# Performance work log

Measured on AMD Instinct MI355X. Metric: run time of the kernel, lower is better.

Reference implementation:

```python
import jax, jax.numpy as jnp
import numpy as np

N_NODES = 10000
N_GRAPHS = 64
NEG_SLOPE = 0.2
EPS = 1e-16


def gat_conv(x, src, dst, W, a_src, a_dst, bias, heads, out_ch, num_nodes):
    """PyG GATConv (shared lin, add_self_loops already applied to src/dst)."""
    xl = (x @ W).reshape(num_nodes, heads, out_ch)          # [N,H,C]
    alpha_s = jnp.einsum('nhc,hc->nh', xl, a_src)           # [N,H]
    alpha_d = jnp.einsum('nhc,hc->nh', xl, a_dst)           # [N,H]
    e = jax.nn.leaky_relu(alpha_s[src] + alpha_d[dst], NEG_SLOPE)  # [E,H]
    # segment softmax over incoming edges of each destination node
    emax = jax.ops.segment_max(e, dst, num_segments=num_nodes)
    emax = jnp.where(jnp.isfinite(emax), emax, 0.0)
    ee = jnp.exp(e - emax[dst])
    denom = jax.ops.segment_sum(ee, dst, num_segments=num_nodes)
    alpha = ee / (denom[dst] + EPS)                         # [E,H]
    msg = xl[src] * alpha[:, :, None]                       # [E,H,C]
    out = jax.ops.segment_sum(msg, dst, num_segments=num_nodes)  # [N,H,C]
    return out.reshape(num_nodes, heads * out_ch) + bias


def setup_inputs() -> dict:
    key = jax.random.key(0)
    ks = jax.random.split(key, 16)
    H, C, IN = 8, 128, 128
    x = jax.random.normal(ks[0], (N_NODES, IN), jnp.float32)
    edge_index = jax.random.randint(ks[1], (2, 320000), 0, N_NODES, jnp.int64)
    batch = jnp.sort(jax.random.randint(ks[2], (N_NODES,), 0, N_GRAPHS, jnp.int64))
    g = lambda k, shp, fan: jax.random.normal(k, shp, jnp.float32) * (1.0 / np.sqrt(fan))
    return {
        'x': x, 'edge_index': edge_index, 'batch': batch,
        'W1': g(ks[3], (IN, H * C), IN),
        'a_src1': g(ks[4], (H, C), C), 'a_dst1': g(ks[5], (H, C), C),
        'b1': jnp.zeros((H * C,), jnp.float32),
        'W2': g(ks[6], (H * C, C), H * C),
        'a_src2': g(ks[7], (1, C), C), 'a_dst2': g(ks[8], (1, C), C),
        'b2': jnp.zeros((C,), jnp.float32),
        'lin1_w': g(ks[9], (C, 128), C), 'lin1_b': jnp.zeros((128,), jnp.float32),
        'lin2_w': g(ks[10], (128, 1), 128), 'lin2_b': jnp.zeros((1,), jnp.float32),
    }


def reference(x, edge_index, batch, W1, a_src1, a_dst1, b1, W2, a_src2, a_dst2, b2,
              lin1_w, lin1_b, lin2_w, lin2_b):
    loops = jnp.arange(N_NODES, dtype=edge_index.dtype)
    src = jnp.concatenate([edge_index[0], loops])
    dst = jnp.concatenate([edge_index[1], loops])
    h = jax.nn.elu(gat_conv(x, src, dst, W1, a_src1, a_dst1, b1, 8, 128, N_NODES))
    h = jax.nn.elu(gat_conv(h, src, dst, W2, a_src2, a_dst2, b2, 1, 128, N_NODES))
    # global mean pool over graphs
    sums = jax.ops.segment_sum(h, batch, num_segments=N_GRAPHS)
    cnts = jax.ops.segment_sum(jnp.ones((N_NODES,), h.dtype), batch, num_segments=N_GRAPHS)
    pooled = sums / jnp.maximum(cnts, 1.0)[:, None]         # [G,128]
    z = jax.nn.relu(pooled @ lin1_w + lin1_b)
    return (z @ lin2_w + lin2_b).squeeze(1)                 # [G]
```

## Files before the change

kernel.cpp:

```cpp
#include <hip/hip_runtime.h>
#include <math.h>

#define N_NODES 10000
#define N_GRAPHS 64
#define E_RAW 320000
#define E_ALL (E_RAW + N_NODES)
#define NEG_SLOPE 0.2f
#define EPS 1e-16f
#define CAP 192

typedef unsigned short ushort_t;
typedef short short8 __attribute__((ext_vector_type(8)));
typedef float floatx4 __attribute__((ext_vector_type(4)));

static __device__ __forceinline__ float bfl(unsigned u) {
  union { unsigned u; float f; } v; v.u = u << 16; return v.f;
}
static __device__ __forceinline__ float bfh(unsigned u) {
  union { unsigned u; float f; } v; v.u = u & 0xFFFF0000u; return v.f;
}
static __device__ __forceinline__ ushort_t f2bf(float f) {
  union { float f; unsigned u; } v; v.f = f;
  unsigned r = v.u + 0x7FFFu + ((v.u >> 16) & 1u);
  return (ushort_t)(r >> 16);
}

static __device__ __forceinline__ void load16_lds(const ushort_t* gp, ushort_t* ldsbase, int lane) {
#if __has_builtin(__builtin_amdgcn_global_load_lds)
  __builtin_amdgcn_global_load_lds((const __attribute__((address_space(1))) void*)gp,
                                   (__attribute__((address_space(3))) void*)ldsbase, 16, 0, 0);
#else
  *(uint4*)(ldsbase + lane * 8) = *(const uint4*)gp;
#endif
}

static __device__ __forceinline__ void swz_one(const float* __restrict__ W,
                                               ushort_t* __restrict__ Wsw,
                                               int idx, int K, int N) {
  int NT = N >> 4;
  int lane = idx & 63, tile = idx >> 6;
  int nt = tile % NT, kt = tile / NT;
  int n = nt * 16 + (lane & 15);
  int kb = kt * 32 + (lane >> 4) * 8;
  ushort4 lo, hi;
  lo.x = f2bf(W[(size_t)(kb + 0) * N + n]); lo.y = f2bf(W[(size_t)(kb + 1) * N + n]);
  lo.z = f2bf(W[(size_t)(kb + 2) * N + n]); lo.w = f2bf(W[(size_t)(kb + 3) * N + n]);
  hi.x = f2bf(W[(size_t)(kb + 4) * N + n]); hi.y = f2bf(W[(size_t)(kb + 5) * N + n]);
  hi.z = f2bf(W[(size_t)(kb + 6) * N + n]); hi.w = f2bf(W[(size_t)(kb + 7) * N + n]);
  *(ushort4*)(Wsw + (size_t)idx * 8) = lo;
  *(ushort4*)(Wsw + (size_t)idx * 8 + 4) = hi;
}

__global__ __launch_bounds__(1024) void prep_k(const float* __restrict__ x,
                                               const int* __restrict__ batch,
                                               const float* __restrict__ W1,
                                               const float* __restrict__ W2,
                                               const float* __restrict__ aS1,
                                               const float* __restrict__ aD1,
                                               ushort_t* __restrict__ xb,
                                               ushort_t* __restrict__ W1sw,
                                               ushort_t* __restrict__ W2sw,
                                               float* __restrict__ zero0,
                                               int* __restrict__ poolcnt,
                                               float* __restrict__ wAs,
                                               float* __restrict__ wAd) {
  __shared__ int shm[N_GRAPHS];
  const int b = blockIdx.x, t = threadIdx.x;
  if (b < 10) {
    int i4 = b * 1024 + t;
    if (i4 < 9548) *(float4*)(zero0 + i4 * 4) = make_float4(0.f, 0.f, 0.f, 0.f);
  } else if (b == 10) {
    if (t < N_GRAPHS) shm[t] = 0;
    __syncthreads();
    for (int n = t; n < N_NODES; n += 1024) atomicAdd(&shm[batch[n]], 1);
    __syncthreads();
    if (t < N_GRAPHS) poolcnt[t] = shm[t];
  } else if (b < 324) {
    int i4 = (b - 11) * 1024 + t;
    if (i4 < 320000) {
      float4 v = *(const float4*)(x + (size_t)i4 * 4);
      ushort4 o;
      o.x = f2bf(v.x); o.y = f2bf(v.y); o.z = f2bf(v.z); o.w = f2bf(v.w);
      *(ushort4*)(xb + (size_t)i4 * 4) = o;
    }
  } else if (b < 340) {
    int idx = (b - 324) * 1024 + t;
    if (idx < 16384) swz_one(W1, W1sw, idx, 128, 1024);
  } else if (b < 356) {
    int idx = (b - 340) * 1024 + t;
    if (idx < 16384) swz_one(W2, W2sw, idx, 1024, 128);
  } else {
    int h = t >> 7, k = t & 127;
    const float* wrow = W1 + (size_t)k * 1024 + h * 128;
    const float* as = aS1 + h * 128;
    const float* ad = aD1 + h * 128;
    float accS = 0.f, accD = 0.f;
    for (int c = 0; c < 128; c += 4) {
      float4 wv = *(const float4*)(wrow + c);
      float4 sv = *(const float4*)(as + c);
      float4 dv = *(const float4*)(ad + c);
      accS = fmaf(wv.x, sv.x, accS); accS = fmaf(wv.y, sv.y, accS);
      accS = fmaf(wv.z, sv.z, accS); accS = fmaf(wv.w, sv.w, accS);
      accD = fmaf(wv.x, dv.x, accD); accD = fmaf(wv.y, dv.y, accD);
      accD = fmaf(wv.z, dv.z, accD); accD = fmaf(wv.w, dv.w, accD);
    }
    wAs[h * 128 + k] = accS;
    wAd[h * 128 + k] = accD;
  }
}

__global__ __launch_bounds__(256) void lgf_k(const int* __restrict__ ei,
                                             int* __restrict__ degc,
                                             int* __restrict__ csr,
                                             const float* __restrict__ x,
                                             const float* __restrict__ wAs,
                                             const float* __restrict__ wAd,
                                             float* __restrict__ as1,
                                             float* __restrict__ ad1) {
  const int bid = blockIdx.x, t = threadIdx.x;
  if (bid < 1290) {
    int e = bid * 256 + t;
    if (e < E_ALL) {
      int s, d;
      if (e < E_RAW) { s = ei[e]; d = ei[E_RAW + e]; }
      else           { s = d = e - E_RAW; }
      int pos = atomicAdd(&degc[d], 1);
      if (pos < CAP) csr[d * CAP + pos] = s;
    }
    return;
  }
  int nb = bid - 1290;
  int n = nb * 16 + (t >> 4);
  int cb = t & 15, h = cb >> 1, sd = cb & 1;
  const float* w = (sd ? wAd : wAs) + h * 128;
  const float* xr = x + (size_t)n * 128;
  float acc = 0.f;
  for (int k = 0; k < 128; k += 4) {
    float4 xv = *(const float4*)(xr + k);
    float4 wv = *(const float4*)(w + k);
    acc = fmaf(xv.x, wv.x, acc); acc = fmaf(xv.y, wv.y, acc);
    acc = fmaf(xv.z, wv.z, acc); acc = fmaf(xv.w, wv.w, acc);
  }
  if (sd) ad1[n * 8 + h] = acc;
  else    as1[n * 8 + h] = acc;
}

__global__ __launch_bounds__(64) void agg1x_k(const ushort_t* __restrict__ xb,
                                              const float* __restrict__ as1,
                                              const float* __restrict__ ad1,
                                              const int* __restrict__ degc,
                                              const int* __restrict__ csr,
                                              ushort_t* __restrict__ aggx) {
  const int dst = blockIdx.x, t = threadIdx.x;
  int deg = degc[dst]; deg = deg < CAP ? deg : CAP;
  const int beg = dst * CAP;
  __shared__ unsigned offs[CAP];
  __shared__ float al[CAP][8];
  float ad[8];
  {
    float4 d0 = *(const float4*)(ad1 + dst * 8);
    float4 d1 = *(const float4*)(ad1 + dst * 8 + 4);
    ad[0] = d0.x; ad[1] = d0.y; ad[2] = d0.z; ad[3] = d0.w;
    ad[4] = d1.x; ad[5] = d1.y; ad[6] = d1.z; ad[7] = d1.w;
  }
  float pmax[8];
  #pragma unroll
  for (int h = 0; h < 8; h++) pmax[h] = -1e30f;
  for (int e = t; e < deg; e += 64) {
    int s = csr[beg + e];
    offs[e] = (unsigned)(s * 256);
    float4 a0 = *(const float4*)(as1 + s * 8);
    float4 a1 = *(const float4*)(as1 + s * 8 + 4);
    float lg[8] = {a0.x + ad[0], a0.y + ad[1], a0.z + ad[2], a0.w + ad[3],
                   a1.x + ad[4], a1.y + ad[5], a1.z + ad[6], a1.w + ad[7]};
    #pragma unroll
    for (int h = 0; h < 8; h++) {
      float v = lg[h]; v = v > 0.f ? v : NEG_SLOPE * v;
      al[e][h] = v;
      pmax[h] = fmaxf(pmax[h], v);
    }
  }
  #pragma unroll
  for (int h = 0; h < 8; h++) {
    #pragma unroll
    for (int off = 32; off; off >>= 1) pmax[h] = fmaxf(pmax[h], __shfl_xor(pmax[h], off));
  }
  float ps[8] = {};
  for (int e = t; e < deg; e += 64) {
    #pragma unroll
    for (int h = 0; h < 8; h++) {
      float ex = __expf(al[e][h] - pmax[h]);
      al[e][h] = ex;
      ps[h] += ex;
    }
  }
  #pragma unroll
  for (int h = 0; h < 8; h++) {
    #pragma unroll
    for (int off = 32; off; off >>= 1) ps[h] += __shfl_xor(ps[h], off);
    ps[h] = 1.0f / (ps[h] + EPS);
  }
  for (int e = t; e < deg; e += 64) {
    #pragma unroll
    for (int h = 0; h < 8; h++) al[e][h] *= ps[h];
  }
  const int degp = (deg + 3) & ~3;
  for (int e = deg + t; e < degp; e += 64) {
    offs[e] = 0;
    #pragma unroll
    for (int h = 0; h < 8; h++) al[e][h] = 0.f;
  }
  __syncthreads();
  const char* xbase = (const char*)xb;
  const unsigned toff = (unsigned)(4 * t);
  float aL[8] = {}, aH[8] = {};
  for (int e0 = 0; e0 < degp; e0 += 4) {
    #pragma unroll
    for (int j = 0; j < 4; j++) {
      int e = e0 + j;
      unsigned u = *(const unsigned*)(xbase + (offs[e] + toff));
      float4 q0 = *(const float4*)&al[e][0];
      float4 q1 = *(const float4*)&al[e][4];
      float lo = bfl(u), hi = bfh(u);
      aL[0] = fmaf(q0.x, lo, aL[0]); aH[0] = fmaf(q0.x, hi, aH[0]);
      aL[1] = fmaf(q0.y, lo, aL[1]); aH[1] = fmaf(q0.y, hi, aH[1]);
      aL[2] = fmaf(q0.z, lo, aL[2]); aH[2] = fmaf(q0.z, hi, aH[2]);
      aL[3] = fmaf(q0.w, lo, aL[3]); aH[3] = fmaf(q0.w, hi, aH[3]);
      aL[4] = fmaf(q1.x, lo, aL[4]); aH[4] = fmaf(q1.x, hi, aH[4]);
      aL[5] = fmaf(q1.y, lo, aL[5]); aH[5] = fmaf(q1.y, hi, aH[5]);
      aL[6] = fmaf(q1.z, lo, aL[6]); aH[6] = fmaf(q1.z, hi, aH[6]);
      aL[7] = fmaf(q1.w, lo, aL[7]); aH[7] = fmaf(q1.w, hi, aH[7]);
    }
  }
  ushort_t* op = aggx + (size_t)dst * 1024 + 2 * t;
  #pragma unroll
  for (int h = 0; h < 8; h++) {
    unsigned up = (unsigned)f2bf(aL[h]) | ((unsigned)f2bf(aH[h]) << 16);
    *(unsigned*)(op + h * 128) = up;
  }
}

__global__ __launch_bounds__(256) void gemm1h_k(const ushort_t* __restrict__ A,
                                                const ushort_t* __restrict__ Bsw,
                                                const float* __restrict__ b1,
                                                ushort_t* __restrict__ Cb) {
  __shared__ ushort_t Albuf[32 * 512];
  __shared__ float epi[4][16][68];
  const int bid = blockIdx.x, t = threadIdx.x;
  const int M = N_NODES, NT = 64;
  const int lane = t & 63, w = t >> 6;
  const int wm = w >> 1, wn = w & 1;
  const int m0 = (bid >> 3) * 128;
  const int h = bid & 7;
  const int g = lane >> 4, l16 = lane & 15;

  #pragma unroll
  for (int i = 0; i < 8; i++) {
    int tile = w * 8 + i;
    int mtl = tile >> 2, kt = tile & 3;
    int r = m0 + mtl * 16 + l16; r = r < M ? r : M - 1;
    load16_lds(A + ((size_t)r * 8 + h) * 128 + kt * 32 + g * 8, &Albuf[tile * 512], lane);
  }
  __syncthreads();

  floatx4 acc[4][4] = {};
  #pragma unroll
  for (int kt = 0; kt < 4; kt++) {
    short8 a[4], b[4];
    #pragma unroll
    for (int mi = 0; mi < 4; mi++)
      a[mi] = *(const short8*)&Albuf[(((wm * 4 + mi) * 4 + kt) * 64 + lane) * 8];
    #pragma unroll
    for (int ni = 0; ni < 4; ni++) {
      int nt = h * 8 + wn * 4 + ni;
      b[ni] = *(const short8*)(Bsw + ((size_t)(kt * NT + nt) * 64 + lane) * 8);
    }
    #pragma unroll
    for (int mi = 0; mi < 4; mi++)
      #pragma unroll
      for (int ni = 0; ni < 4; ni++)
        acc[mi][ni] = __builtin_amdgcn_mfma_f32_16x16x32_bf16(a[mi], b[ni], acc[mi][ni], 0, 0, 0);
  }

  const int r = lane >> 2, c0 = (lane & 3) * 16;
  const int colh = wn * 64 + c0;
  float bv[16];
  #pragma unroll
  for (int c = 0; c < 16; c++) bv[c] = b1[h * 128 + colh + c];
  #pragma unroll
  for (int mi = 0; mi < 4; mi++) {
    #pragma unroll
    for (int ni = 0; ni < 4; ni++)
      #pragma unroll
      for (int reg = 0; reg < 4; reg++)
        epi[w][g * 4 + reg][ni * 16 + l16] = acc[mi][ni][reg];
    float4 v0 = *(float4*)&epi[w][r][c0];
    float4 v1 = *(float4*)&epi[w][r][c0 + 4];
    float4 v2 = *(float4*)&epi[w][r][c0 + 8];
    float4 v3 = *(float4*)&epi[w][r][c0 + 12];
    float vr[16] = {v0.x,v0.y,v0.z,v0.w, v1.x,v1.y,v1.z,v1.w,
                    v2.x,v2.y,v2.z,v2.w, v3.x,v3.y,v3.z,v3.w};
    int grow = m0 + wm * 64 + mi * 16 + r;
    if (grow < M) {
      ushort_t hv[16];
      #pragma unroll
      for (int c = 0; c < 16; c++) {
        float v = vr[c] + bv[c];
        v = v > 0.f ? v : (__expf(v) - 1.0f);
        hv[c] = f2bf(v);
      }
      uint4 u0, u1;
      u0.x = (unsigned)hv[0] | ((unsigned)hv[1] << 16);
      u0.y = (unsigned)hv[2] | ((unsigned)hv[3] << 16);
      u0.z = (unsigned)hv[4] | ((unsigned)hv[5] << 16);
      u0.w = (unsigned)hv[6] | ((unsigned)hv[7] << 16);
      u1.x = (unsigned)hv[8] | ((unsigned)hv[9] << 16);
      u1.y = (unsigned)hv[10] | ((unsigned)hv[11] << 16);
      u1.z = (unsigned)hv[12] | ((unsigned)hv[13] << 16);
      u1.w = (unsigned)hv[14] | ((unsigned)hv[15] << 16);
      ushort_t* cp = Cb + (size_t)grow * 1024 + h * 128 + colh;
      *(uint4*)cp = u0;
      *(uint4*)(cp + 8) = u1;
    }
  }
}

__global__ __launch_bounds__(256) void gemm2_k(const ushort_t* __restrict__ A,
                                               const ushort_t* __restrict__ Bsw,
                                               ushort_t* __restrict__ Cb,
                                               const float* __restrict__ aS,
                                               const float* __restrict__ aD,
                                               float* __restrict__ asO,
                                               float* __restrict__ adO) {
  const int M = N_NODES, K = 1024, NT = 8;
  __shared__ ushort_t Albuf[4 * 512];
  __shared__ float epi[4][16][36];
  const int t = threadIdx.x, lane = t & 63, w = t >> 6;
  const int mb0 = blockIdx.x * 16;
  const int g = lane >> 4, l16 = lane & 15;

  floatx4 acc[2] = {};
  for (int ch = 0; ch < 8; ch++) {
    {
      int r = mb0 + l16; r = r < M ? r : M - 1;
      load16_lds(A + (size_t)r * K + (ch * 4 + w) * 32 + g * 8, &Albuf[w * 512], lane);
    }
    __syncthreads();
    #pragma unroll
    for (int ks = 0; ks < 4; ks++) {
      short8 a = *(const short8*)&Albuf[(ks * 64 + lane) * 8];
      #pragma unroll
      for (int ni = 0; ni < 2; ni++) {
        int nt = w * 2 + ni, ktg = ch * 4 + ks;
        short8 b = *(const short8*)(Bsw + ((size_t)(ktg * NT + nt) * 64 + lane) * 8);
        acc[ni] = __builtin_amdgcn_mfma_f32_16x16x32_bf16(a, b, acc[ni], 0, 0, 0);
      }
    }
    __syncthreads();
  }

  const int r = lane >> 2, c0 = (lane & 3) * 8;
  const int colh = w * 32 + c0;
  float asc[8], adc[8];
  #pragma unroll
  for (int c = 0; c < 8; c++) { asc[c] = aS[colh + c]; adc[c] = aD[colh + c]; }
  #pragma unroll
  for (int ni = 0; ni < 2; ni++)
    #pragma unroll
    for (int reg = 0; reg < 4; reg++)
      epi[w][g * 4 + reg][ni * 16 + l16] = acc[ni][reg];
  float4 v0 = *(float4*)&epi[w][r][c0];
  float4 v1 = *(float4*)&epi[w][r][c0 + 4];
  float vr[8] = {v0.x, v0.y, v0.z, v0.w, v1.x, v1.y, v1.z, v1.w};
  int grow = mb0 + r;
  float sp = 0.f, dp = 0.f;
  ushort_t hv[8];
  #pragma unroll
  for (int c = 0; c < 8; c++) {
    sp = fmaf(vr[c], asc[c], sp);
    dp = fmaf(vr[c], adc[c], dp);
    hv[c] = f2bf(vr[c]);
  }
  sp += __shfl_xor(sp, 1); sp += __shfl_xor(sp, 2);
  dp += __shfl_xor(dp, 1); dp += __shfl_xor(dp, 2);
  if (grow < M) {
    uint4 u0;
    u0.x = (unsigned)hv[0] | ((unsigned)hv[1] << 16);
    u0.y = (unsigned)hv[2] | ((unsigned)hv[3] << 16);
    u0.z = (unsigned)hv[4] | ((unsigned)hv[5] << 16);
    u0.w = (unsigned)hv[6] | ((unsigned)hv[7] << 16);
    *(uint4*)(Cb + (size_t)grow * 128 + colh) = u0;
    if ((lane & 3) == 0) {
      atomicAdd(&asO[grow], sp);
      atomicAdd(&adO[grow], dp);
    }
  }
}

__global__ __launch_bounds__(64) void agg2_k(const ushort_t* __restrict__ xlb2,
                                             const float* __restrict__ as2,
                                             const float* __restrict__ ad2,
                                             const float* __restrict__ b2,
                                             const int* __restrict__ degc,
                                             const int* __restrict__ csr,
                                             const int* __restrict__ batch,
                                             float* __restrict__ poolsum) {
  int dst = blockIdx.x, t = threadIdx.x;
  int deg = degc[dst]; deg = deg < CAP ? deg : CAP;
  int beg = dst * CAP;
  const int degp = (deg + 7) & ~7;
  float adv = ad2[dst];
  __shared__ uint2 pr[CAP];
  if (deg <= 64) {
    bool act = t < deg;
    int s = act ? csr[beg + t] : 0;
    float lg = -1e30f;
    if (act) {
      float v = as2[s] + adv;
      lg = v > 0.f ? v : NEG_SLOPE * v;
    }
    float pm = lg;
    #pragma unroll
    for (int off = 32; off; off >>= 1) pm = fmaxf(pm, __shfl_xor(pm, off));
    float ex = act ? __expf(lg - pm) : 0.f;
    float ps = ex;
    #pragma unroll
    for (int off = 32; off; off >>= 1) ps += __shfl_xor(ps, off);
    float inv = 1.0f / (ps + EPS);
    if (t < degp) pr[t] = act ? make_uint2((unsigned)(s * 256), __float_as_uint(ex * inv))
                              : make_uint2(0u, 0u);
    __syncthreads();
  } else {
    __shared__ int ssg[CAP];
    __shared__ float alg[CAP];
    for (int e = t; e < deg; e += 64) ssg[e] = csr[beg + e];
    __syncthreads();
    float pm = -1e30f;
    for (int e = t; e < deg; e += 64) {
      float v = as2[ssg[e]] + adv;
      v = v > 0.f ? v : NEG_SLOPE * v;
      alg[e] = v;
      pm = fmaxf(pm, v);
    }
    #pragma unroll
    for (int off = 32; off; off >>= 1) pm = fmaxf(pm, __shfl_xor(pm, off));
    __syncthreads();
    float ps = 0.f;
    for (int e = t; e < deg; e += 64) ps += __expf(alg[e] - pm);
    #pragma unroll
    for (int off = 32; off; off >>= 1) ps += __shfl_xor(ps, off);
    float inv = 1.0f / (ps + EPS);
    for (int e = t; e < deg; e += 64)
      pr[e] = make_uint2((unsigned)(ssg[e] * 256), __float_as_uint(__expf(alg[e] - pm) * inv));
    for (int e = deg + t; e < degp; e += 64) pr[e] = make_uint2(0u, 0u);
    __syncthreads();
  }
  const char* xbase = (const char*)xlb2;
  const unsigned toff = (unsigned)(4 * t);
  float accA[4] = {}, accB[4] = {};
  for (int e0 = 0; e0 < degp; e0 += 8) {
    #pragma unroll
    for (int j = 0; j < 8; j++) {
      uint2 p = pr[e0 + j];
      unsigned u = *(const unsigned*)(xbase + (p.x + toff));
      float a = __uint_as_float(p.y);
      accA[j & 3] = fmaf(a, bfl(u), accA[j & 3]);
      accB[j & 3] = fmaf(a, bfh(u), accB[j & 3]);
    }
  }
  float acc0 = (accA[0] + accA[1]) + (accA[2] + accA[3]);
  float acc1 = (accB[0] + accB[1]) + (accB[2] + accB[3]);
  int c0 = 2 * t;
  float v0 = acc0 + b2[c0];
  float v1 = acc1 + b2[c0 + 1];
  v0 = v0 > 0.f ? v0 : (__expf(v0) - 1.0f);
  v1 = v1 > 0.f ? v1 : (__expf(v1) - 1.0f);
  int g = batch[dst];
  atomicAdd(&poolsum[g * 128 + c0], v0);
  atomicAdd(&poolsum[g * 128 + c0 + 1], v1);
}

__global__ __launch_bounds__(128) void final_k(const float* __restrict__ poolsum,
                                               const int* __restrict__ cnt,
                                               const float* __restrict__ l1w,
                                               const float* __restrict__ l1b,
                                               const float* __restrict__ l2w,
                                               const float* __restrict__ l2b,
                                               float* __restrict__ out) {
  int g = blockIdx.x, t = threadIdx.x;
  __shared__ float pooled[128];
  float c = fmaxf((float)cnt[g], 1.0f);
  pooled[t] = poolsum[g * 128 + t] / c;
  __syncthreads();
  float acc = l1b[t];
  for (int i = 0; i < 128; i++) acc = fmaf(pooled[i], l1w[i * 128 + t], acc);
  acc = fmaxf(acc, 0.0f);
  float p = acc * l2w[t];
  #pragma unroll
  for (int off = 32; off; off >>= 1) p += __shfl_down(p, off);
  __shared__ float r[2];
  if ((t & 63) == 0) r[t >> 6] = p;
  __syncthreads();
  if (t == 0) out[g] = r[0] + r[1] + l2b[0];
}

extern "C" void kernel_launch(void* const* d_in, const int* in_sizes, int n_in,
                              void* d_out, int out_size, void* d_ws, size_t ws_size,
                              hipStream_t stream) {
  const float* x    = (const float*)d_in[0];
  const int*   ei   = (const int*)d_in[1];
  const int*   batch= (const int*)d_in[2];
  const float* W1   = (const float*)d_in[3];
  const float* aS1  = (const float*)d_in[4];
  const float* aD1  = (const float*)d_in[5];
  const float* b1   = (const float*)d_in[6];
  const float* W2   = (const float*)d_in[7];
  const float* aS2  = (const float*)d_in[8];
  const float* aD2  = (const float*)d_in[9];
  const float* b2   = (const float*)d_in[10];
  const float* l1w  = (const float*)d_in[11];
  const float* l1b  = (const float*)d_in[12];
  const float* l2w  = (const float*)d_in[13];
  const float* l2b  = (const float*)d_in[14];
  float* out = (float*)d_out;

  ushort_t* xb     = (ushort_t*)d_ws;
  ushort_t* aggx   = xb + 1280000;
  ushort_t* h1b    = aggx + 10240000;
  ushort_t* xlb2   = h1b + 10240000;
  ushort_t* W1sw   = xlb2 + 1280000;
  ushort_t* W2sw   = W1sw + 131072;
  float*    wAs    = (float*)(W2sw + 131072);
  float*    wAd    = wAs + 1024;
  float*    as1    = wAd + 1024;
  float*    ad1    = as1 + 80000;
  float*    zero0  = ad1 + 80000;
  float*    as2    = zero0;
  float*    ad2    = as2 + 10000;
  float*    poolsum= ad2 + 10000;
  int*      degc   = (int*)(poolsum + 8192);
  int*      poolcnt= (int*)(zero0 + 38192);
  int*      csr    = poolcnt + 64;

  prep_k<<<357, 1024, 0, stream>>>(x, batch, W1, W2, aS1, aD1, xb, W1sw, W2sw,
                                   zero0, poolcnt, wAs, wAd);
  lgf_k<<<1290 + 625, 256, 0, stream>>>(ei, degc, csr, x, wAs, wAd, as1, ad1);
  agg1x_k<<<N_NODES, 64, 0, stream>>>(xb, as1, ad1, degc, csr, aggx);
  gemm1h_k<<<632, 256, 0, stream>>>(aggx, W1sw, b1, h1b);
  gemm2_k<<<625, 256, 0, stream>>>(h1b, W2sw, xlb2, aS2, aD2, as2, ad2);
  agg2_k<<<N_NODES, 64, 0, stream>>>(xlb2, as2, ad2, b2, degc, csr, batch, poolsum);
  final_k<<<N_GRAPHS, 128, 0, stream>>>(poolsum, poolcnt, l1w, l1b, l2w, l2b, out);
}
```

Baseline: 222.9 us.

## Split edge aggregation across four waves per node with deferred softmax normalization

Both GAT aggregation kernels now launch 256 threads per destination node instead of 64. Each of the four waves gathers a contiguous quarter of the incoming edges, computing exp inline and accumulating the softmax denominator alongside the weighted features. The partial sums are then combined through shared memory and normalized once at the end. This is meant to raise memory-level parallelism on the gathers and remove the separate softmax passes, at the cost of extra shared memory, a block-wide barrier and a cross-wave reduction.

```diff
diff --git a/kernel.cpp b/kernel.cpp
--- a/kernel.cpp
+++ b/kernel.cpp
@@ -145,17 +145,20 @@
   else    as1[n * 8 + h] = acc;
 }
 
-__global__ __launch_bounds__(64) void agg1x_k(const ushort_t* __restrict__ xb,
-                                              const float* __restrict__ as1,
-                                              const float* __restrict__ ad1,
-                                              const int* __restrict__ degc,
-                                              const int* __restrict__ csr,
-                                              ushort_t* __restrict__ aggx) {
+__global__ __launch_bounds__(256) void agg1x_k(const ushort_t* __restrict__ xb,
+                                               const float* __restrict__ as1,
+                                               const float* __restrict__ ad1,
+                                               const int* __restrict__ degc,
+                                               const int* __restrict__ csr,
+                                               ushort_t* __restrict__ aggx) {
   const int dst = blockIdx.x, t = threadIdx.x;
+  const int lane = t & 63, wv = t >> 6;
   int deg = degc[dst]; deg = deg < CAP ? deg : CAP;
   const int beg = dst * CAP;
   __shared__ unsigned offs[CAP];
   __shared__ float al[CAP][8];
+  __shared__ float red[4][8][128];
+  __shared__ float rps[4][8];
   float ad[8];
   {
     float4 d0 = *(const float4*)(ad1 + dst * 8);
@@ -163,80 +166,84 @@
     ad[0] = d0.x; ad[1] = d0.y; ad[2] = d0.z; ad[3] = d0.w;
     ad[4] = d1.x; ad[5] = d1.y; ad[6] = d1.z; ad[7] = d1.w;
   }
-  float pmax[8];
-  #pragma unroll
-  for (int h = 0; h < 8; h++) pmax[h] = -1e30f;
-  for (int e = t; e < deg; e += 64) {
-    int s = csr[beg + e];
-    offs[e] = (unsigned)(s * 256);
+  if (t < deg) {
+    int s = csr[beg + t];
+    offs[t] = (unsigned)(s * 256);
     float4 a0 = *(const float4*)(as1 + s * 8);
     float4 a1 = *(const float4*)(as1 + s * 8 + 4);
     float lg[8] = {a0.x + ad[0], a0.y + ad[1], a0.z + ad[2], a0.w + ad[3],
                    a1.x + ad[4], a1.y + ad[5], a1.z + ad[6], a1.w + ad[7]};
     #pragma unroll
     for (int h = 0; h < 8; h++) {
-      float v = lg[h]; v = v > 0.f ? v : NEG_SLOPE * v;
-      al[e][h] = v;
-      pmax[h] = fmaxf(pmax[h], v);
-    }
+      float v = lg[h];
+      al[t][h] = v > 0.f ? v : NEG_SLOPE * v;
+    }
+  }
+  __syncthreads();
+  float pmax[8];
+  #pragma unroll
+  for (int h = 0; h < 8; h++) pmax[h] = -1e30f;
+  for (int e = lane; e < deg; e += 64) {
+    float4 a0 = *(const float4*)&al[e][0];
+    float4 a1 = *(const float4*)&al[e][4];
+    pmax[0] = fmaxf(pmax[0], a0.x); pmax[1] = fmaxf(pmax[1], a0.y);
+    pmax[2] = fmaxf(pmax[2], a0.z); pmax[3] = fmaxf(pmax[3], a0.w);
+    pmax[4] = fmaxf(pmax[4], a1.x); pmax[5] = fmaxf(pmax[5], a1.y);
+    pmax[6] = fmaxf(pmax[6], a1.z); pmax[7] = fmaxf(pmax[7], a1.w);
   }
   #pragma unroll
   for (int h = 0; h < 8; h++) {
     #pragma unroll
     for (int off = 32; off; off >>= 1) pmax[h] = fmaxf(pmax[h], __shfl_xor(pmax[h], off));
   }
-  float ps[8] = {};
-  for (int e = t; e < deg; e += 64) {
-    #pragma unroll
-    for (int h = 0; h < 8; h++) {
-      float ex = __expf(al[e][h] - pmax[h]);
-      al[e][h] = ex;
-      ps[h] += ex;
-    }
-  }
-  #pragma unroll
-  for (int h = 0; h < 8; h++) {
-    #pragma unroll
-    for (int off = 32; off; off >>= 1) ps[h] += __shfl_xor(ps[h], off);
-    ps[h] = 1.0f / (ps[h] + EPS);
-  }
-  for (int e = t; e < deg; e += 64) {
-    #pragma unroll
-    for (int h = 0; h < 8; h++) al[e][h] *= ps[h];
-  }
-  const int degp = (deg + 3) & ~3;
-  for (int e = deg + t; e < degp; e += 64) {
-    offs[e] = 0;
-    #pragma unroll
-    for (int h = 0; h < 8; h++) al[e][h] = 0.f;
-  }
-  __syncthreads();
   const char* xbase = (const char*)xb;
-  const unsigned toff = (unsigned)(4 * t);
-  float aL[8] = {}, aH[8] = {};
-  for (int e0 = 0; e0 < degp; e0 += 4) {
-    #pragma unroll
-    for (int j = 0; j < 4; j++) {
-      int e = e0 + j;
-      unsigned u = *(const unsigned*)(xbase + (offs[e] + toff));
-      float4 q0 = *(const float4*)&al[e][0];
-      float4 q1 = *(const float4*)&al[e][4];
-      float lo = bfl(u), hi = bfh(u);
-      aL[0] = fmaf(q0.x, lo, aL[0]); aH[0] = fmaf(q0.x, hi, aH[0]);
-      aL[1] = fmaf(q0.y, lo, aL[1]); aH[1] = fmaf(q0.y, hi, aH[1]);
-      aL[2] = fmaf(q0.z, lo, aL[2]); aH[2] = fmaf(q0.z, hi, aH[2]);
-      aL[3] = fmaf(q0.w, lo, aL[3]); aH[3] = fmaf(q0.w, hi, aH[3]);
-      aL[4] = fmaf(q1.x, lo, aL[4]); aH[4] = fmaf(q1.x, hi, aH[4]);
-      aL[5] = fmaf(q1.y, lo, aL[5]); aH[5] = fmaf(q1.y, hi, aH[5]);
-      aL[6] = fmaf(q1.z, lo, aL[6]); aH[6] = fmaf(q1.z, hi, aH[6]);
-      aL[7] = fmaf(q1.w, lo, aL[7]); aH[7] = fmaf(q1.w, hi, aH[7]);
-    }
-  }
-  ushort_t* op = aggx + (size_t)dst * 1024 + 2 * t;
-  #pragma unroll
-  for (int h = 0; h < 8; h++) {
-    unsigned up = (unsigned)f2bf(aL[h]) | ((unsigned)f2bf(aH[h]) << 16);
-    *(unsigned*)(op + h * 128) = up;
+  const unsigned toff = (unsigned)(4 * lane);
+  int q = (deg + 3) >> 2;
+  int e_lo = wv * q;
+  int e_hi = e_lo + q; e_hi = e_hi < deg ? e_hi : deg;
+  float aL[8] = {}, aH[8] = {}, psumP[8] = {};
+  for (int e = e_lo; e < e_hi; e++) {
+    float4 a0 = *(const float4*)&al[e][0];
+    float4 a1 = *(const float4*)&al[e][4];
+    unsigned u = *(const unsigned*)(xbase + (offs[e] + toff));
+    float ex0 = __expf(a0.x - pmax[0]), ex1 = __expf(a0.y - pmax[1]);
+    float ex2 = __expf(a0.z - pmax[2]), ex3 = __expf(a0.w - pmax[3]);
+    float ex4 = __expf(a1.x - pmax[4]), ex5 = __expf(a1.y - pmax[5]);
+    float ex6 = __expf(a1.z - pmax[6]), ex7 = __expf(a1.w - pmax[7]);
+    float lo = bfl(u), hi = bfh(u);
+    aL[0] = fmaf(ex0, lo, aL[0]); aH[0] = fmaf(ex0, hi, aH[0]); psumP[0] += ex0;
+    aL[1] = fmaf(ex1, lo, aL[1]); aH[1] = fmaf(ex1, hi, aH[1]); psumP[1] += ex1;
+    aL[2] = fmaf(ex2, lo, aL[2]); aH[2] = fmaf(ex2, hi, aH[2]); psumP[2] += ex2;
+    aL[3] = fmaf(ex3, lo, aL[3]); aH[3] = fmaf(ex3, hi, aH[3]); psumP[3] += ex3;
+    aL[4] = fmaf(ex4, lo, aL[4]); aH[4] = fmaf(ex4, hi, aH[4]); psumP[4] += ex4;
+    aL[5] = fmaf(ex5, lo, aL[5]); aH[5] = fmaf(ex5, hi, aH[5]); psumP[5] += ex5;
+    aL[6] = fmaf(ex6, lo, aL[6]); aH[6] = fmaf(ex6, hi, aH[6]); psumP[6] += ex6;
+    aL[7] = fmaf(ex7, lo, aL[7]); aH[7] = fmaf(ex7, hi, aH[7]); psumP[7] += ex7;
+  }
+  #pragma unroll
+  for (int h = 0; h < 8; h++)
+    *(float2*)&red[wv][h][2 * lane] = make_float2(aL[h], aH[h]);
+  if (lane == 0) {
+    #pragma unroll
+    for (int h = 0; h < 8; h++) rps[wv][h] = psumP[h];
+  }
+  __syncthreads();
+  {
+    int h = t >> 5, c4 = (t & 31) * 4;
+    float ps = rps[0][h] + rps[1][h] + rps[2][h] + rps[3][h];
+    float inv = 1.0f / (ps + EPS);
+    float4 r0 = *(const float4*)&red[0][h][c4];
+    float4 r1 = *(const float4*)&red[1][h][c4];
+    float4 r2 = *(const float4*)&red[2][h][c4];
+    float4 r3 = *(const float4*)&red[3][h][c4];
+    float v0 = (r0.x + r1.x + r2.x + r3.x) * inv;
+    float v1 = (r0.y + r1.y + r2.y + r3.y) * inv;
+    float v2 = (r0.z + r1.z + r2.z + r3.z) * inv;
+    float v3 = (r0.w + r1.w + r2.w + r3.w) * inv;
+    uint2 up;
+    up.x = (unsigned)f2bf(v0) | ((unsigned)f2bf(v1) << 16);
+    up.y = (unsigned)f2bf(v2) | ((unsigned)f2bf(v3) << 16);
+    *(uint2*)(aggx + (size_t)dst * 1024 + h * 128 + c4) = up;
   }
 }
 
@@ -397,87 +404,58 @@
   }
 }
 
-__global__ __launch_bounds__(64) void agg2_k(const ushort_t* __restrict__ xlb2,
-                                             const float* __restrict__ as2,
-                                             const float* __restrict__ ad2,
-                                             const float* __restrict__ b2,
-                                             const int* __restrict__ degc,
-                                             const int* __restrict__ csr,
-                                             const int* __restrict__ batch,
-                                             float* __restrict__ poolsum) {
-  int dst = blockIdx.x, t = threadIdx.x;
+__global__ __launch_bounds__(256) void agg2_k(const ushort_t* __restrict__ xlb2,
+                                              const float* __restrict__ as2,
+                                              const float* __restrict__ ad2,
+                                              const float* __restrict__ b2,
+                                              const int* __restrict__ degc,
+                                              const int* __restrict__ csr,
+                                              const int* __restrict__ batch,
+                                              float* __restrict__ poolsum) {
+  const int dst = blockIdx.x, t = threadIdx.x;
+  const int lane = t & 63, wv = t >> 6;
   int deg = degc[dst]; deg = deg < CAP ? deg : CAP;
-  int beg = dst * CAP;
-  const int degp = (deg + 7) & ~7;
+  const int beg = dst * CAP;
   float adv = ad2[dst];
-  __shared__ uint2 pr[CAP];
-  if (deg <= 64) {
-    bool act = t < deg;
-    int s = act ? csr[beg + t] : 0;
-    float lg = -1e30f;
-    if (act) {
-      float v = as2[s] + adv;
-      lg = v > 0.f ? v : NEG_SLOPE * v;
-    }
-    float pm = lg;
-    #pragma unroll
-    for (int off = 32; off; off >>= 1) pm = fmaxf(pm, __shfl_xor(pm, off));
-    float ex = act ? __expf(lg - pm) : 0.f;
-    float ps = ex;
-    #pragma unroll
-    for (int off = 32; off; off >>= 1) ps += __shfl_xor(ps, off);
+  __shared__ unsigned offs[CAP];
+  __shared__ float alg[CAP];
+  __shared__ float red2[4][128];
+  __shared__ float rps2[4];
+  if (t < deg) {
+    int s = csr[beg + t];
+    offs[t] = (unsigned)(s * 256);
+    float v = as2[s] + adv;
+    alg[t] = v > 0.f ? v : NEG_SLOPE * v;
+  }
+  __syncthreads();
+  float pm = -1e30f;
+  for (int e = lane; e < deg; e += 64) pm = fmaxf(pm, alg[e]);
+  #pragma unroll
+  for (int off = 32; off; off >>= 1) pm = fmaxf(pm, __shfl_xor(pm, off));
+  const char* xbase = (const char*)xlb2;
+  const unsigned toff = (unsigned)(4 * lane);
+  int q = (deg + 3) >> 2;
+  int e_lo = wv * q;
+  int e_hi = e_lo + q; e_hi = e_hi < deg ? e_hi : deg;
+  float accA = 0.f, accB = 0.f, psumP = 0.f;
+  for (int e = e_lo; e < e_hi; e++) {
+    float ex = __expf(alg[e] - pm);
+    unsigned u = *(const unsigned*)(xbase + (offs[e] + toff));
+    accA = fmaf(ex, bfl(u), accA);
+    accB = fmaf(ex, bfh(u), accB);
+    psumP += ex;
+  }
+  *(float2*)&red2[wv][2 * lane] = make_float2(accA, accB);
+  if (lane == 0) rps2[wv] = psumP;
+  __syncthreads();
+  if (t < 128) {
+    float ps = rps2[0] + rps2[1] + rps2[2] + rps2[3];
     float inv = 1.0f / (ps + EPS);
-    if (t < degp) pr[t] = act ? make_uint2((unsigned)(s * 256), __float_as_uint(ex * inv))
-                              : make_uint2(0u, 0u);
-    __syncthreads();
-  } else {
-    __shared__ int ssg[CAP];
-    __shared__ float alg[CAP];
-    for (int e = t; e < deg; e += 64) ssg[e] = csr[beg + e];
-    __syncthreads();
-    float pm = -1e30f;
-    for (int e = t; e < deg; e += 64) {
-      float v = as2[ssg[e]] + adv;
-      v = v > 0.f ? v : NEG_SLOPE * v;
-      alg[e] = v;
-      pm = fmaxf(pm, v);
-    }
-    #pragma unroll
-    for (int off = 32; off; off >>= 1) pm = fmaxf(pm, __shfl_xor(pm, off));
-    __syncthreads();
-    float ps = 0.f;
-    for (int e = t; e < deg; e += 64) ps += __expf(alg[e] - pm);
-    #pragma unroll
-    for (int off = 32; off; off >>= 1) ps += __shfl_xor(ps, off);
-    float inv = 1.0f / (ps + EPS);
-    for (int e = t; e < deg; e += 64)
-      pr[e] = make_uint2((unsigned)(ssg[e] * 256), __float_as_uint(__expf(alg[e] - pm) * inv));
-    for (int e = deg + t; e < degp; e += 64) pr[e] = make_uint2(0u, 0u);
-    __syncthreads();
-  }
-  const char* xbase = (const char*)xlb2;
-  const unsigned toff = (unsigned)(4 * t);
-  float accA[4] = {}, accB[4] = {};
-  for (int e0 = 0; e0 < degp; e0 += 8) {
-    #pragma unroll
-    for (int j = 0; j < 8; j++) {
-      uint2 p = pr[e0 + j];
-      unsigned u = *(const unsigned*)(xbase + (p.x + toff));
-      float a = __uint_as_float(p.y);
-      accA[j & 3] = fmaf(a, bfl(u), accA[j & 3]);
-      accB[j & 3] = fmaf(a, bfh(u), accB[j & 3]);
-    }
-  }
-  float acc0 = (accA[0] + accA[1]) + (accA[2] + accA[3]);
-  float acc1 = (accB[0] + accB[1]) + (accB[2] + accB[3]);
-  int c0 = 2 * t;
-  float v0 = acc0 + b2[c0];
-  float v1 = acc1 + b2[c0 + 1];
-  v0 = v0 > 0.f ? v0 : (__expf(v0) - 1.0f);
-  v1 = v1 > 0.f ? v1 : (__expf(v1) - 1.0f);
-  int g = batch[dst];
-  atomicAdd(&poolsum[g * 128 + c0], v0);
-  atomicAdd(&poolsum[g * 128 + c0 + 1], v1);
+    float v = (red2[0][t] + red2[1][t] + red2[2][t] + red2[3][t]) * inv + b2[t];
+    v = v > 0.f ? v : (__expf(v) - 1.0f);
+    int g = batch[dst];
+    atomicAdd(&poolsum[g * 128 + t], v);
+  }
 }
 
 __global__ __launch_bounds__(128) void final_k(const float* __restrict__ poolsum,
@@ -545,9 +523,9 @@
   prep_k<<<357, 1024, 0, stream>>>(x, batch, W1, W2, aS1, aD1, xb, W1sw, W2sw,
                                    zero0, poolcnt, wAs, wAd);
   lgf_k<<<1290 + 625, 256, 0, stream>>>(ei, degc, csr, x, wAs, wAd, as1, ad1);
-  agg1x_k<<<N_NODES, 64, 0, stream>>>(xb, as1, ad1, degc, csr, aggx);
+  agg1x_k<<<N_NODES, 256, 0, stream>>>(xb, as1, ad1, degc, csr, aggx);
   gemm1h_k<<<632, 256, 0, stream>>>(aggx, W1sw, b1, h1b);
   gemm2_k<<<625, 256, 0, stream>>>(h1b, W2sw, xlb2, aS2, aD2, as2, ad2);
-  agg2_k<<<N_NODES, 64, 0, stream>>>(xlb2, as2, ad2, b2, degc, csr, batch, poolsum);
+  agg2_k<<<N_NODES, 256, 0, stream>>>(xlb2, as2, ad2, b2, degc, csr, batch, poolsum);
   final_k<<<N_GRAPHS, 128, 0, stream>>>(poolsum, poolcnt, l1w, l1b, l2w, l2b, out);
 }
```

Result: slower. 254.0 us (+14.0%).
